# Kernel tuning notes

Hardware: AMD Instinct MI355X
Metric: run time of the kernel (lower is better)

The kernel has to match this reference:

```python
import jax, jax.numpy as jnp
import numpy as np

DIM = 2048
NUM_HEADS = 16
HEAD_DIM = DIM // NUM_HEADS
FF_MULT = 2
ROPE_BASE = 10000.0
EPS = 1e-6


def _rmsnorm(x, g):
    return x * jax.lax.rsqrt(jnp.mean(x * x, axis=-1, keepdims=True) + EPS) * g


def _rope_tables(seq_len):
    half = HEAD_DIM // 2
    inv_freq = 1.0 / (ROPE_BASE ** (2.0 * jnp.arange(half, dtype=jnp.float32) / HEAD_DIM))
    angles = jnp.arange(seq_len, dtype=jnp.float32)[:, None] * inv_freq[None, :]  # (S, half)
    return jnp.cos(angles), jnp.sin(angles)


def _apply_rope(x, cos, sin):
    # x: (B, H, S, D); cos/sin: (S, D/2). Interleaved pairs (RoFormer form).
    x_even = x[..., 0::2]
    x_odd = x[..., 1::2]
    c = cos[None, None].astype(x.dtype)
    s = sin[None, None].astype(x.dtype)
    rot_even = x_even * c - x_odd * s
    rot_odd = x_odd * c + x_even * s
    return jnp.stack([rot_even, rot_odd], axis=-1).reshape(x.shape)


def setup_inputs() -> dict:
    key = jax.random.key(0)
    ks = jax.random.split(key, 7)
    B, S = 2, 2048
    scale = 1.0 / np.sqrt(DIM)
    return {
        "x": jax.random.normal(ks[0], (B, S, DIM), dtype=jnp.float32),
        "w_qkv": jax.random.normal(ks[1], (DIM, 3 * DIM), dtype=jnp.float32) * scale,
        "w_out": jax.random.normal(ks[2], (DIM, DIM), dtype=jnp.float32) * scale,
        "w_fc": jax.random.normal(ks[3], (DIM, DIM * FF_MULT), dtype=jnp.float32) * scale,
        "w_proj": jax.random.normal(ks[4], (DIM * FF_MULT, DIM), dtype=jnp.float32) / np.sqrt(DIM * FF_MULT),
        "g_in": jnp.ones((DIM,), dtype=jnp.float32),
        "g_ff": jnp.ones((DIM,), dtype=jnp.float32),
    }


def reference(x, w_qkv, w_out, w_fc, w_proj, g_in, g_ff):
    B, S, D = x.shape
    # --- attention branch ---
    h = _rmsnorm(x, g_in)
    qkv = h @ w_qkv  # (B, S, 3D)
    q, k, v = jnp.split(qkv, 3, axis=-1)
    def heads(t):
        return t.reshape(B, S, NUM_HEADS, HEAD_DIM).transpose(0, 2, 1, 3)
    q, k, v = heads(q), heads(k), heads(v)  # (B, H, S, Dh)
    cos, sin = _rope_tables(S)
    q = _apply_rope(q, cos, sin)
    k = _apply_rope(k, cos, sin)
    scores = jnp.einsum("bhqd,bhkd->bhqk", q, k) / jnp.asarray(np.sqrt(HEAD_DIM), x.dtype)
    causal = jnp.tril(jnp.ones((S, S), dtype=bool))
    scores = jnp.where(causal[None, None], scores, jnp.asarray(-jnp.inf, scores.dtype))
    attn = jax.nn.softmax(scores, axis=-1)
    out = jnp.einsum("bhqk,bhkd->bhqd", attn, v)  # (B, H, S, Dh)
    out = out.transpose(0, 2, 1, 3).reshape(B, S, D)
    x = x + out @ w_out
    # --- feed-forward branch ---
    h = _rmsnorm(x, g_ff)
    x = x + jax.nn.gelu(h @ w_fc) @ w_proj
    return x


if __name__ == "__main__":
    inp = setup_inputs()
    y = reference(**inp)
    print(y.shape, y.dtype)
```

## Files before the change

### kernel.cpp

```cpp
#include <hip/hip_runtime.h>
#include <math.h>

typedef __bf16 bf16x8 __attribute__((ext_vector_type(8)));
typedef float  f32x4  __attribute__((ext_vector_type(4)));

#define DEV __device__ __forceinline__

DEV void gload16(const void* g, void* l) {
  __builtin_amdgcn_global_load_lds(
      (const __attribute__((address_space(1))) void*)g,
      (__attribute__((address_space(3))) void*)l, 16, 0, 0);
}

__global__ __launch_bounds__(256) void transpose_cvt(
    const float* __restrict__ in, __bf16* __restrict__ outT, int R, int C) {
  __shared__ float t[32][33];
  const int c0 = blockIdx.x * 32, r0 = blockIdx.y * 32;
  const int tx = threadIdx.x, ty = threadIdx.y;
#pragma unroll
  for (int i = 0; i < 4; i++)
    t[ty + 8 * i][tx] = in[(size_t)(r0 + ty + 8 * i) * C + c0 + tx];
  __syncthreads();
#pragma unroll
  for (int i = 0; i < 4; i++)
    outT[(size_t)(c0 + ty + 8 * i) * R + r0 + tx] = (__bf16)t[tx][ty + 8 * i];
}

__global__ __launch_bounds__(256) void rmsnorm_kernel(
    const float* __restrict__ x, const float* __restrict__ g, __bf16* __restrict__ out) {
  const int r = blockIdx.x, t = threadIdx.x;
  const float4* xr = (const float4*)(x + (size_t)r * 2048);
  float4 a = xr[2 * t], b = xr[2 * t + 1];
  float ss = a.x * a.x + a.y * a.y + a.z * a.z + a.w * a.w +
             b.x * b.x + b.y * b.y + b.z * b.z + b.w * b.w;
#pragma unroll
  for (int mk = 1; mk < 64; mk <<= 1) ss += __shfl_xor(ss, mk);
  __shared__ float red[4];
  if ((t & 63) == 0) red[t >> 6] = ss;
  __syncthreads();
  const float sc = rsqrtf((red[0] + red[1] + red[2] + red[3]) * (1.0f / 2048.0f) + 1e-6f);
  const float4* gr = (const float4*)g;
  float4 ga = gr[2 * t], gb = gr[2 * t + 1];
  bf16x8 ov;
  ov[0] = (__bf16)(a.x * sc * ga.x); ov[1] = (__bf16)(a.y * sc * ga.y);
  ov[2] = (__bf16)(a.z * sc * ga.z); ov[3] = (__bf16)(a.w * sc * ga.w);
  ov[4] = (__bf16)(b.x * sc * gb.x); ov[5] = (__bf16)(b.y * sc * gb.y);
  ov[6] = (__bf16)(b.z * sc * gb.z); ov[7] = (__bf16)(b.w * sc * gb.w);
  *(bf16x8*)(out + (size_t)r * 2048 + t * 8) = ov;
}

template <int EPI>
__global__ __launch_bounds__(256) void gemm_bt(
    const __bf16* __restrict__ A, const __bf16* __restrict__ BT,
    void* __restrict__ Cout, const float* __restrict__ res, int M, int N, int K) {
  __shared__ char lds[32768];
  char* As = lds;
  char* Bs = lds + 16384;
  const int tid = threadIdx.x;
  const int lane = tid & 63;
  const int bn = blockIdx.x, bm = blockIdx.y;
  const int wm = tid >> 7, wn = (tid >> 6) & 1;

  f32x4 acc[4][4];
#pragma unroll
  for (int i = 0; i < 4; i++)
#pragma unroll
    for (int j = 0; j < 4; j++) acc[i][j] = (f32x4){0.f, 0.f, 0.f, 0.f};

  const size_t strideA = (size_t)K * 2;
  const char* ga[4];
  const char* gb[4];
#pragma unroll
  for (int t = 0; t < 4; t++) {
    int gg = t * 256 + tid;
    int row = gg >> 3, slot = gg & 7;
    ga[t] = (const char*)A + (size_t)(bm * 128 + row) * strideA + ((slot ^ (row & 7)) << 4);
    gb[t] = (const char*)BT + (size_t)(bn * 128 + row) * strideA + ((slot ^ (row & 7)) << 4);
  }

  for (int k0 = 0; k0 < K; k0 += 64) {
    __syncthreads();
#pragma unroll
    for (int t = 0; t < 4; t++) {
      int gg = t * 256 + tid;
      gload16(ga[t], As + gg * 16);
      gload16(gb[t], Bs + gg * 16);
      ga[t] += 128;
      gb[t] += 128;
    }
    __syncthreads();
#pragma unroll
    for (int kk = 0; kk < 2; kk++) {
      bf16x8 a[4], b[4];
      const int c16 = kk * 4 + (lane >> 4);
#pragma unroll
      for (int i = 0; i < 4; i++) {
        int ra = wm * 64 + i * 16 + (lane & 15);
        a[i] = *(const bf16x8*)(As + ra * 128 + ((c16 ^ (ra & 7)) << 4));
        int rb = wn * 64 + i * 16 + (lane & 15);
        b[i] = *(const bf16x8*)(Bs + rb * 128 + ((c16 ^ (rb & 7)) << 4));
      }
#pragma unroll
      for (int i = 0; i < 4; i++)
#pragma unroll
        for (int j = 0; j < 4; j++)
          acc[i][j] = __builtin_amdgcn_mfma_f32_16x16x32_bf16(a[i], b[j], acc[i][j], 0, 0, 0);
    }
  }

#pragma unroll
  for (int i = 0; i < 4; i++)
#pragma unroll
    for (int j = 0; j < 4; j++)
#pragma unroll
      for (int r = 0; r < 4; r++) {
        int row = bm * 128 + wm * 64 + i * 16 + ((lane >> 4) << 2) + r;
        int col = bn * 128 + wn * 64 + j * 16 + (lane & 15);
        size_t idx = (size_t)row * N + col;
        float v = acc[i][j][r];
        if (EPI == 0) {
          ((__bf16*)Cout)[idx] = (__bf16)v;
        } else if (EPI == 1) {
          ((float*)Cout)[idx] = v + res[idx];
        } else {
          float u = 0.7978845608028654f * (v + 0.044715f * v * v * v);
          ((__bf16*)Cout)[idx] = (__bf16)(0.5f * v * (1.0f + tanhf(u)));
        }
      }
}

#define MMQ(IB, JB, AR, BR)                                                   \
  __builtin_amdgcn_s_setprio(1);                                              \
  _Pragma("unroll") for (int i = 0; i < 4; i++)                               \
      _Pragma("unroll") for (int j = 0; j < 2; j++)                           \
          _Pragma("unroll") for (int kk = 0; kk < 2; kk++)                    \
              acc[(IB)*4 + i][(JB)*2 + j] =                                   \
      __builtin_amdgcn_mfma_f32_16x16x32_bf16(                                \
          AR[i][kk], BR[j][kk], acc[(IB)*4 + i][(JB)*2 + j], 0, 0, 0);        \
  __builtin_amdgcn_s_setprio(0);

template <int EPI>
__global__ __launch_bounds__(512, 2) void gemm256(
    const __bf16* __restrict__ A, const __bf16* __restrict__ BT,
    void* __restrict__ Cout, const float* __restrict__ res, int M, int N, int K) {
  __shared__ char lds[131072];
  const int tid = threadIdx.x, lane = tid & 63, w = tid >> 6;
  const int wm = w >> 2, wn = w & 3;
  const int bn = blockIdx.x, bm = blockIdx.y;

  f32x4 acc[8][4];
#pragma unroll
  for (int i = 0; i < 8; i++)
#pragma unroll
    for (int j = 0; j < 4; j++) acc[i][j] = (f32x4){0.f, 0.f, 0.f, 0.f};

  const size_t strideA = (size_t)K * 2;
  const int r0 = tid >> 3, s0 = tid & 7;
  const int r1 = r0 + 64;
  const char* Ab0 = (const char*)A + (size_t)(bm * 256) * strideA;
  const char* Bb0 = (const char*)BT + (size_t)(bn * 256) * strideA;

  auto stage = [&](int isB, int h, int kt, int buf) {
    const char* g = (isB ? Bb0 : Ab0) + (size_t)(h * 128) * strideA + (size_t)kt * 128;
    char* d = lds + isB * 65536 + buf * 32768 + h * 16384;
    gload16(g + (size_t)r0 * strideA + ((s0 ^ (r0 & 7)) << 4), d + tid * 16);
    gload16(g + (size_t)r1 * strideA + ((s0 ^ (r1 & 7)) << 4), d + (tid + 512) * 16);
  };
  auto ldA = [&](bf16x8 (&a)[4][2], int buf, int bank) {
    const char* base = lds + buf * 32768 + wm * 16384;
#pragma unroll
    for (int i = 0; i < 4; i++)
#pragma unroll
      for (int kk = 0; kk < 2; kk++) {
        int rl = bank * 64 + i * 16 + (lane & 15);
        int c16 = kk * 4 + (lane >> 4);
        a[i][kk] = *(const bf16x8*)(base + rl * 128 + ((c16 ^ (rl & 7)) << 4));
      }
  };
  auto ldB = [&](bf16x8 (&b)[2][2], int buf, int jb) {
    const char* base = lds + 65536 + buf * 32768 + (wn >> 1) * 16384;
#pragma unroll
    for (int j = 0; j < 2; j++)
#pragma unroll
      for (int kk = 0; kk < 2; kk++) {
        int rl = (wn & 1) * 64 + jb * 32 + j * 16 + (lane & 15);
        int c16 = kk * 4 + (lane >> 4);
        b[j][kk] = *(const bf16x8*)(base + rl * 128 + ((c16 ^ (rl & 7)) << 4));
      }
  };

  const int NT = K >> 6;
  stage(1, 0, 0, 0); stage(1, 1, 0, 0); stage(0, 0, 0, 0); stage(0, 1, 0, 0);
  stage(1, 0, 1, 1); stage(1, 1, 1, 1); stage(0, 0, 1, 1); stage(0, 1, 1, 1);
  asm volatile("s_waitcnt vmcnt(6)" ::: "memory");
  __builtin_amdgcn_s_barrier();

  bf16x8 a[4][2], b0[2][2], b1[2][2];
  for (int it = 0; it < (NT >> 1); ++it) {
    const int e = 2 * it;
    const int ep = (e + 2 < NT) ? e + 2 : NT - 1;
    const int op = (e + 3 < NT) ? e + 3 : NT - 1;
    ldA(a, 0, 0); ldB(b0, 0, 0);
    __builtin_amdgcn_s_barrier();
    MMQ(0, 0, a, b0);
    __builtin_amdgcn_s_barrier();
    ldB(b1, 0, 1);
    __builtin_amdgcn_s_barrier();
    MMQ(0, 1, a, b1);
    __builtin_amdgcn_s_barrier();
    ldA(a, 0, 1); stage(1, 0, ep, 0);
    __builtin_amdgcn_s_barrier();
    MMQ(1, 1, a, b1);
    __builtin_amdgcn_s_barrier();
    stage(1, 1, ep, 0);
    asm volatile("s_waitcnt vmcnt(4)" ::: "memory");
    __builtin_amdgcn_s_barrier();
    MMQ(1, 0, a, b0);
    __builtin_amdgcn_s_barrier();
    ldA(a, 1, 0); ldB(b0, 1, 0); stage(0, 0, ep, 0);
    __builtin_amdgcn_s_barrier();
    MMQ(0, 0, a, b0);
    __builtin_amdgcn_s_barrier();
    ldB(b1, 1, 1); stage(0, 1, ep, 0);
    __builtin_amdgcn_s_barrier();
    MMQ(0, 1, a, b1);
    __builtin_amdgcn_s_barrier();
    ldA(a, 1, 1); stage(1, 0, op, 1);
    __builtin_amdgcn_s_barrier();
    MMQ(1, 1, a, b1);
    __builtin_amdgcn_s_barrier();
    stage(1, 1, op, 1); stage(0, 0, op, 1); stage(0, 1, op, 1);
    asm volatile("s_waitcnt vmcnt(6)" ::: "memory");
    __builtin_amdgcn_s_barrier();
    MMQ(1, 0, a, b0);
    __builtin_amdgcn_s_barrier();
  }
  asm volatile("s_waitcnt vmcnt(0)" ::: "memory");

#pragma unroll
  for (int i = 0; i < 8; i++)
#pragma unroll
    for (int j = 0; j < 4; j++)
#pragma unroll
      for (int r = 0; r < 4; r++) {
        int row = bm * 256 + wm * 128 + i * 16 + ((lane >> 4) << 2) + r;
        int col = bn * 256 + wn * 64 + j * 16 + (lane & 15);
        size_t idx = (size_t)row * N + col;
        float v = acc[i][j][r];
        if (EPI == 0) {
          ((__bf16*)Cout)[idx] = (__bf16)v;
        } else if (EPI == 1) {
          ((float*)Cout)[idx] = v + res[idx];
        } else {
          float u = 0.7978845608028654f * (v + 0.044715f * v * v * v);
          ((__bf16*)Cout)[idx] = (__bf16)(0.5f * v * (1.0f + tanhf(u)));
        }
      }
}

__global__ __launch_bounds__(256) void rope_tables(float* __restrict__ tab) {
  const int idx = blockIdx.x * 256 + threadIdx.x;
  const int s = idx >> 6, j = idx & 63;
  const float inv = powf(10000.0f, -(float)j / 64.0f);
  const float a = (float)s * inv;
  tab[idx] = cosf(a);
  tab[131072 + idx] = sinf(a);
}

__global__ __launch_bounds__(256) void rope_apply(
    const __bf16* __restrict__ qkv, const float* __restrict__ tab,
    __bf16* __restrict__ qr, __bf16* __restrict__ kr) {
  const int idx = blockIdx.x * 256 + threadIdx.x;
  const int j = idx & 63;
  const int h = (idx >> 6) & 15;
  const int s = (idx >> 10) & 2047;
  const int b = idx >> 21;
  const float c = tab[(s << 6) + j], sn = tab[131072 + (s << 6) + j];
  const size_t qi = ((size_t)(b * 2048 + s)) * 6144 + h * 128 + 2 * j;
  const size_t qo = ((size_t)((b * 16 + h) * 2048 + s)) * 128 + 2 * j;
  {
    float e = (float)qkv[qi], o = (float)qkv[qi + 1];
    qr[qo] = (__bf16)(e * c - o * sn);
    qr[qo + 1] = (__bf16)(o * c + e * sn);
  }
  {
    float e = (float)qkv[qi + 2048], o = (float)qkv[qi + 2048 + 1];
    kr[qo] = (__bf16)(e * c - o * sn);
    kr[qo + 1] = (__bf16)(o * c + e * sn);
  }
}

__global__ __launch_bounds__(256) void v_transpose(
    const __bf16* __restrict__ qkv, __bf16* __restrict__ vt) {
  __shared__ __bf16 t[32][33];
  const int s0 = blockIdx.x * 32, d0 = blockIdx.y * 32, bh = blockIdx.z;
  const int b = bh >> 4, h = bh & 15;
  const int tx = threadIdx.x, ty = threadIdx.y;
#pragma unroll
  for (int i = 0; i < 4; i++)
    t[ty + 8 * i][tx] =
        qkv[((size_t)(b * 2048 + s0 + ty + 8 * i)) * 6144 + 4096 + h * 128 + d0 + tx];
  __syncthreads();
#pragma unroll
  for (int i = 0; i < 4; i++)
    vt[((size_t)bh * 128 + d0 + ty + 8 * i) * 2048 + s0 + tx] = t[tx][ty + 8 * i];
}

__global__ __launch_bounds__(512) void flash_attn(
    const __bf16* __restrict__ qg, const __bf16* __restrict__ kg,
    const __bf16* __restrict__ vtg, __bf16* __restrict__ og) {
  __shared__ char lds[81920];
  const int tid = threadIdx.x, lane = tid & 63, w = tid >> 6;
  const int h = blockIdx.y, b = blockIdx.z;
  const int bh = b * 16 + h;
  const __bf16* qb = qg + (size_t)bh * 2048 * 128;
  const char* kbb = (const char*)(kg + (size_t)bh * 2048 * 128);
  const char* vbb = (const char*)(vtg + (size_t)bh * 128 * 2048);
  char* Pw = lds + 65536 + w * 2048;

  const char* gK[2];
  const char* gV[2];
#pragma unroll
  for (int t = 0; t < 2; t++) {
    int gg = t * 512 + tid;
    int rk = gg >> 4, sk = gg & 15;
    gK[t] = kbb + rk * 256 + ((sk ^ (rk & 15)) << 4);
    int rv = gg >> 3, sv = gg & 7;
    gV[t] = vbb + rv * 4096 + ((sv ^ (rv & 7)) << 4);
  }

  const float SL2E = 0.08838834764831845f * 1.4426950408889634f;

  auto stageKV = [&](int kt, int buf) {
#pragma unroll
    for (int t = 0; t < 2; t++) {
      int gg = t * 512 + tid;
      gload16(gK[t] + (size_t)kt * 16384, lds + buf * 16384 + gg * 16);
      gload16(gV[t] + (size_t)kt * 128, lds + 32768 + buf * 16384 + gg * 16);
    }
  };

  auto run_qtile = [&](int qt) {
    const int qrow0 = qt * 128 + w * 16;
    bf16x8 qf[4];
#pragma unroll
    for (int c = 0; c < 4; c++) {
      bf16x8 raw = *(const bf16x8*)(qb + (size_t)(qrow0 + (lane & 15)) * 128 +
                                    c * 32 + ((lane >> 4) << 3));
#pragma unroll
      for (int e = 0; e < 8; e++) qf[c][e] = (__bf16)((float)raw[e] * SL2E);
    }
    float m[4], lsp[4];
    f32x4 o[8];
#pragma unroll
    for (int r = 0; r < 4; r++) { m[r] = -__builtin_inff(); lsp[r] = 0.f; }
#pragma unroll
    for (int n = 0; n < 8; n++) o[n] = (f32x4){0.f, 0.f, 0.f, 0.f};

    const int NKT = 2 * qt + 2;
    stageKV(0, 0);

    for (int kt = 0; kt < NKT; kt++) {
      const int cur = kt & 1;
      const char* Ks = lds + cur * 16384;
      const char* Vs = lds + 32768 + cur * 16384;
      if (kt < NKT - 1) {
        stageKV(kt + 1, cur ^ 1);
        asm volatile("s_waitcnt vmcnt(4)" ::: "memory");
      } else {
        asm volatile("s_waitcnt vmcnt(0)" ::: "memory");
      }
      __builtin_amdgcn_s_barrier();

      f32x4 s[4];
      __builtin_amdgcn_s_setprio(1);
#pragma unroll
      for (int n = 0; n < 4; n++) {
        s[n] = (f32x4){0.f, 0.f, 0.f, 0.f};
#pragma unroll
        for (int c = 0; c < 4; c++) {
          int krow = n * 16 + (lane & 15);
          int c16 = c * 4 + (lane >> 4);
          bf16x8 kf = *(const bf16x8*)(Ks + krow * 256 + ((c16 ^ (krow & 15)) << 4));
          s[n] = __builtin_amdgcn_mfma_f32_16x16x32_bf16(qf[c], kf, s[n], 0, 0, 0);
        }
      }
      __builtin_amdgcn_s_setprio(0);

      if (kt * 64 + 63 > qrow0) {
#pragma unroll
        for (int r = 0; r < 4; r++) {
          const int qrow = qrow0 + ((lane >> 4) << 2) + r;
#pragma unroll
          for (int n = 0; n < 4; n++) {
            int col = kt * 64 + n * 16 + (lane & 15);
            if (col > qrow) s[n][r] = -__builtin_inff();
          }
        }
      }

      float tmx[4];
#pragma unroll
      for (int r = 0; r < 4; r++)
        tmx[r] = fmaxf(fmaxf(s[0][r], s[1][r]), fmaxf(s[2][r], s[3][r]));
      bool hot = (tmx[0] > m[0] + 8.f) | (tmx[1] > m[1] + 8.f) |
                 (tmx[2] > m[2] + 8.f) | (tmx[3] > m[3] + 8.f);
      if (__any(hot)) {
        float fc[4];
#pragma unroll
        for (int r = 0; r < 4; r++) {
          float gmx = tmx[r];
#pragma unroll
          for (int mk = 1; mk < 16; mk <<= 1) gmx = fmaxf(gmx, __shfl_xor(gmx, mk));
          float nm = fmaxf(m[r], gmx);
          fc[r] = __builtin_amdgcn_exp2f(m[r] - nm);
          m[r] = nm;
          lsp[r] *= fc[r];
        }
#pragma unroll
        for (int n = 0; n < 8; n++) {
          o[n][0] *= fc[0]; o[n][1] *= fc[1]; o[n][2] *= fc[2]; o[n][3] *= fc[3];
        }
      }

      float p[4][4];
#pragma unroll
      for (int r = 0; r < 4; r++) {
        float sum = 0.f;
#pragma unroll
        for (int n = 0; n < 4; n++) {
          float pv = __builtin_amdgcn_exp2f(s[n][r] - m[r]);
          p[n][r] = pv;
          sum += pv;
        }
        lsp[r] += sum;
      }

#pragma unroll
      for (int n = 0; n < 4; n++)
#pragma unroll
        for (int r = 0; r < 4; r++) {
          int prow = ((lane >> 4) << 2) + r;
          int col = n * 16 + (lane & 15);
          int ch = col >> 3;
          *(__bf16*)(Pw + prow * 128 + ((ch ^ (prow & 7)) << 4) + ((col & 7) << 1)) =
              (__bf16)p[n][r];
        }

      __builtin_amdgcn_s_setprio(1);
#pragma unroll
      for (int kk = 0; kk < 2; kk++) {
        int prow = lane & 15;
        int pc = kk * 4 + (lane >> 4);
        bf16x8 pf = *(const bf16x8*)(Pw + prow * 128 + ((pc ^ (prow & 7)) << 4));
#pragma unroll
        for (int n = 0; n < 8; n++) {
          int vr = n * 16 + (lane & 15);
          bf16x8 vf = *(const bf16x8*)(Vs + vr * 128 + ((pc ^ (vr & 7)) << 4));
          o[n] = __builtin_amdgcn_mfma_f32_16x16x32_bf16(pf, vf, o[n], 0, 0, 0);
        }
      }
      __builtin_amdgcn_s_setprio(0);
      __builtin_amdgcn_s_barrier();
    }

    float inv[4];
#pragma unroll
    for (int r = 0; r < 4; r++) {
      float ls = lsp[r];
#pragma unroll
      for (int mk = 1; mk < 16; mk <<= 1) ls += __shfl_xor(ls, mk);
      inv[r] = 1.0f / ls;
    }
#pragma unroll
    for (int n = 0; n < 8; n++)
#pragma unroll
      for (int r = 0; r < 4; r++) {
        int qrow = qrow0 + ((lane >> 4) << 2) + r;
        og[(size_t)(b * 2048 + qrow) * 2048 + h * 128 + n * 16 + (lane & 15)] =
            (__bf16)(o[n][r] * inv[r]);
      }
  };

  run_qtile(15 - (int)blockIdx.x);
  run_qtile((int)blockIdx.x);
}

extern "C" void kernel_launch(void* const* d_in, const int* in_sizes, int n_in,
                              void* d_out, int out_size, void* d_ws, size_t ws_size,
                              hipStream_t stream) {
  const float* x = (const float*)d_in[0];
  const float* w_qkv = (const float*)d_in[1];
  const float* w_out = (const float*)d_in[2];
  const float* w_fc = (const float*)d_in[3];
  const float* w_proj = (const float*)d_in[4];
  const float* g_in = (const float*)d_in[5];
  const float* g_ff = (const float*)d_in[6];
  float* out = (float*)d_out;
  char* ws = (char*)d_ws;

  constexpr size_t O_WQKV = 0;
  constexpr size_t O_WOUT = 25165824;
  constexpr size_t O_WFC = 33554432;
  constexpr size_t O_WPROJ = 50331648;
  constexpr size_t O_H = 67108864;
  constexpr size_t O_QKV = 83886080;
  constexpr size_t O_Q = 134217728;
  constexpr size_t O_K = 150994944;
  constexpr size_t O_VT = 167772160;
  constexpr size_t O_TAB = 184549376;
  constexpr size_t O_ATTN = 185597952;
  constexpr size_t O_X1 = 202375168;

  __bf16* wqkvT = (__bf16*)(ws + O_WQKV);
  __bf16* woutT = (__bf16*)(ws + O_WOUT);
  __bf16* wfcT = (__bf16*)(ws + O_WFC);
  __bf16* wprojT = (__bf16*)(ws + O_WPROJ);
  __bf16* h = (__bf16*)(ws + O_H);
  __bf16* qkv = (__bf16*)(ws + O_QKV);
  __bf16* fcact = (__bf16*)(ws + O_QKV);
  __bf16* qr = (__bf16*)(ws + O_Q);
  __bf16* kr = (__bf16*)(ws + O_K);
  __bf16* vt = (__bf16*)(ws + O_VT);
  float* tab = (float*)(ws + O_TAB);
  __bf16* attn = (__bf16*)(ws + O_ATTN);
  float* x1 = (float*)(ws + O_X1);

  const dim3 tb(32, 8);
  transpose_cvt<<<dim3(6144 / 32, 2048 / 32), tb, 0, stream>>>(w_qkv, wqkvT, 2048, 6144);
  transpose_cvt<<<dim3(2048 / 32, 2048 / 32), tb, 0, stream>>>(w_out, woutT, 2048, 2048);
  transpose_cvt<<<dim3(4096 / 32, 2048 / 32), tb, 0, stream>>>(w_fc, wfcT, 2048, 4096);
  transpose_cvt<<<dim3(2048 / 32, 4096 / 32), tb, 0, stream>>>(w_proj, wprojT, 4096, 2048);

  rmsnorm_kernel<<<4096, 256, 0, stream>>>(x, g_in, h);
  gemm256<0><<<dim3(24, 16), 512, 0, stream>>>(h, wqkvT, (void*)qkv, nullptr, 4096, 6144, 2048);
  rope_tables<<<512, 256, 0, stream>>>(tab);
  rope_apply<<<16384, 256, 0, stream>>>(qkv, tab, qr, kr);
  v_transpose<<<dim3(64, 4, 32), tb, 0, stream>>>(qkv, vt);
  flash_attn<<<dim3(8, 16, 2), 512, 0, stream>>>(qr, kr, vt, attn);
  gemm_bt<1><<<dim3(16, 32), 256, 0, stream>>>(attn, woutT, (void*)x1, x, 4096, 2048, 2048);
  rmsnorm_kernel<<<4096, 256, 0, stream>>>(x1, g_ff, h);
  gemm256<2><<<dim3(16, 16), 512, 0, stream>>>(h, wfcT, (void*)fcact, nullptr, 4096, 4096, 2048);
  gemm_bt<1><<<dim3(16, 32), 256, 0, stream>>>(fcact, wprojT, (void*)out, x1, 4096, 2048, 4096);
}
```

Measured before the change: 518.1 us.

## Vectorize weight transpose and RoPE kernels, switch QKV GEMM to gemm_bt

The weight transpose now uses 64x64 tiles with float4 loads and 8-wide bf16 stores. The RoPE apply kernel now processes 8 elements per thread with vector loads and stores. The QKV projection switches from the 256-tile gemm256 kernel to the gemm_bt kernel with a larger grid. These aim to cut memory-transaction overhead in the elementwise kernels, but the GEMM swap could be slower if gemm_bt is less efficient for this shape.

```diff
diff --git a/kernel.cpp b/kernel.cpp
--- a/kernel.cpp
+++ b/kernel.cpp
@@ -14,16 +14,27 @@
 
 __global__ __launch_bounds__(256) void transpose_cvt(
     const float* __restrict__ in, __bf16* __restrict__ outT, int R, int C) {
-  __shared__ float t[32][33];
-  const int c0 = blockIdx.x * 32, r0 = blockIdx.y * 32;
-  const int tx = threadIdx.x, ty = threadIdx.y;
-#pragma unroll
-  for (int i = 0; i < 4; i++)
-    t[ty + 8 * i][tx] = in[(size_t)(r0 + ty + 8 * i) * C + c0 + tx];
+  __shared__ float t[64][65];
+  const int c0 = blockIdx.x * 64, r0 = blockIdx.y * 64;
+  const int tid = threadIdx.x;
+#pragma unroll
+  for (int i = 0; i < 4; i++) {
+    int r = (tid >> 4) + i * 16;
+    int cf = tid & 15;
+    float4 v = *(const float4*)(in + (size_t)(r0 + r) * C + c0 + cf * 4);
+    t[r][cf * 4 + 0] = v.x; t[r][cf * 4 + 1] = v.y;
+    t[r][cf * 4 + 2] = v.z; t[r][cf * 4 + 3] = v.w;
+  }
   __syncthreads();
 #pragma unroll
-  for (int i = 0; i < 4; i++)
-    outT[(size_t)(c0 + ty + 8 * i) * R + r0 + tx] = (__bf16)t[tx][ty + 8 * i];
+  for (int i = 0; i < 2; i++) {
+    int c = (tid >> 3) + i * 32;
+    int r8 = tid & 7;
+    bf16x8 ov;
+#pragma unroll
+    for (int k = 0; k < 8; k++) ov[k] = (__bf16)t[r8 * 8 + k][c];
+    *(bf16x8*)(outT + (size_t)(c0 + c) * R + r0 + r8 * 8) = ov;
+  }
 }
 
 __global__ __launch_bounds__(256) void rmsnorm_kernel(
@@ -271,23 +282,30 @@
     const __bf16* __restrict__ qkv, const float* __restrict__ tab,
     __bf16* __restrict__ qr, __bf16* __restrict__ kr) {
   const int idx = blockIdx.x * 256 + threadIdx.x;
-  const int j = idx & 63;
-  const int h = (idx >> 6) & 15;
-  const int s = (idx >> 10) & 2047;
-  const int b = idx >> 21;
-  const float c = tab[(s << 6) + j], sn = tab[131072 + (s << 6) + j];
-  const size_t qi = ((size_t)(b * 2048 + s)) * 6144 + h * 128 + 2 * j;
-  const size_t qo = ((size_t)((b * 16 + h) * 2048 + s)) * 128 + 2 * j;
-  {
-    float e = (float)qkv[qi], o = (float)qkv[qi + 1];
-    qr[qo] = (__bf16)(e * c - o * sn);
-    qr[qo + 1] = (__bf16)(o * c + e * sn);
-  }
-  {
-    float e = (float)qkv[qi + 2048], o = (float)qkv[qi + 2048 + 1];
-    kr[qo] = (__bf16)(e * c - o * sn);
-    kr[qo + 1] = (__bf16)(o * c + e * sn);
-  }
+  const int ch = idx & 15;
+  const int h = (idx >> 4) & 15;
+  const int s = (idx >> 8) & 2047;
+  const int b = idx >> 19;
+  const float4 c4 = *(const float4*)(tab + (s << 6) + ch * 4);
+  const float4 s4 = *(const float4*)(tab + 131072 + (s << 6) + ch * 4);
+  const float cc[4] = {c4.x, c4.y, c4.z, c4.w};
+  const float ss[4] = {s4.x, s4.y, s4.z, s4.w};
+  const size_t qi = ((size_t)(b * 2048 + s)) * 6144 + h * 128 + ch * 8;
+  const size_t qo = ((size_t)((b * 16 + h) * 2048 + s)) * 128 + ch * 8;
+  bf16x8 vq = *(const bf16x8*)(qkv + qi);
+  bf16x8 vk = *(const bf16x8*)(qkv + qi + 2048);
+  bf16x8 oq, ok;
+#pragma unroll
+  for (int p = 0; p < 4; p++) {
+    float e = (float)vq[2 * p], o = (float)vq[2 * p + 1];
+    oq[2 * p] = (__bf16)(e * cc[p] - o * ss[p]);
+    oq[2 * p + 1] = (__bf16)(o * cc[p] + e * ss[p]);
+    e = (float)vk[2 * p]; o = (float)vk[2 * p + 1];
+    ok[2 * p] = (__bf16)(e * cc[p] - o * ss[p]);
+    ok[2 * p + 1] = (__bf16)(o * cc[p] + e * ss[p]);
+  }
+  *(bf16x8*)(qr + qo) = oq;
+  *(bf16x8*)(kr + qo) = ok;
 }
 
 __global__ __launch_bounds__(256) void v_transpose(
@@ -526,17 +544,16 @@
   __bf16* attn = (__bf16*)(ws + O_ATTN);
   float* x1 = (float*)(ws + O_X1);
 
-  const dim3 tb(32, 8);
-  transpose_cvt<<<dim3(6144 / 32, 2048 / 32), tb, 0, stream>>>(w_qkv, wqkvT, 2048, 6144);
-  transpose_cvt<<<dim3(2048 / 32, 2048 / 32), tb, 0, stream>>>(w_out, woutT, 2048, 2048);
-  transpose_cvt<<<dim3(4096 / 32, 2048 / 32), tb, 0, stream>>>(w_fc, wfcT, 2048, 4096);
-  transpose_cvt<<<dim3(2048 / 32, 4096 / 32), tb, 0, stream>>>(w_proj, wprojT, 4096, 2048);
+  transpose_cvt<<<dim3(96, 32), 256, 0, stream>>>(w_qkv, wqkvT, 2048, 6144);
+  transpose_cvt<<<dim3(32, 32), 256, 0, stream>>>(w_out, woutT, 2048, 2048);
+  transpose_cvt<<<dim3(64, 32), 256, 0, stream>>>(w_fc, wfcT, 2048, 4096);
+  transpose_cvt<<<dim3(32, 64), 256, 0, stream>>>(w_proj, wprojT, 4096, 2048);
 
   rmsnorm_kernel<<<4096, 256, 0, stream>>>(x, g_in, h);
-  gemm256<0><<<dim3(24, 16), 512, 0, stream>>>(h, wqkvT, (void*)qkv, nullptr, 4096, 6144, 2048);
+  gemm_bt<0><<<dim3(48, 32), 256, 0, stream>>>(h, wqkvT, (void*)qkv, nullptr, 4096, 6144, 2048);
   rope_tables<<<512, 256, 0, stream>>>(tab);
-  rope_apply<<<16384, 256, 0, stream>>>(qkv, tab, qr, kr);
-  v_transpose<<<dim3(64, 4, 32), tb, 0, stream>>>(qkv, vt);
+  rope_apply<<<4096, 256, 0, stream>>>(qkv, tab, qr, kr);
+  v_transpose<<<dim3(64, 4, 32), dim3(32, 8), 0, stream>>>(qkv, vt);
   flash_attn<<<dim3(8, 16, 2), 512, 0, stream>>>(qr, kr, vt, attn);
   gemm_bt<1><<<dim3(16, 32), 256, 0, stream>>>(attn, woutT, (void*)x1, x, 4096, 2048, 2048);
   rmsnorm_kernel<<<4096, 256, 0, stream>>>(x1, g_ff, h);
```

Result: faster. 488.6 us (-5.7%).
